# Kernel tuning notes

Measured on AMD Instinct MI355X. Metric: run time of the kernel, lower is better.

Reference implementation:

```python
import jax, jax.numpy as jnp
import numpy as np

ITEM_NUM = 100000
H = 128          # hidden_size
L_PROTO = 500    # number of prototypes
K = 4            # top-k prototypes
SEQ = 50         # max_seq_length
B = 1024
TAO = 0.1
LAMBDA = 0.1
EPS = 1e-5


def layer_norm(x, g, b):
    mu = jnp.mean(x, axis=-1, keepdims=True)
    var = jnp.mean((x - mu) ** 2, axis=-1, keepdims=True)
    return (x - mu) * jax.lax.rsqrt(var + EPS) * g + b


def setup_inputs() -> dict:
    key = jax.random.key(0)
    ks = jax.random.split(key, 12)
    std = 0.02
    item_emb = jax.random.normal(ks[0], (ITEM_NUM, H), jnp.float32) * std
    item_emb = item_emb.at[0].set(0.0)  # padding_idx=0
    pos_emb = jax.random.normal(ks[1], (SEQ + 1, H), jnp.float32) * std
    pos_emb = pos_emb.at[0].set(0.0)    # padding_idx=0 (never hit when len==SEQ)
    proto = jax.random.normal(ks[2], (L_PROTO, H), jnp.float32) * std
    w1 = jax.random.normal(ks[3], (H, H), jnp.float32) * std
    w2 = jax.random.normal(ks[4], (H, 1), jnp.float32) * std
    w3 = jax.random.normal(ks[5], (H, H), jnp.float32) * std
    w4 = jax.random.normal(ks[6], (H, H), jnp.float32) * std
    w5 = jax.random.normal(ks[7], (H, K), jnp.float32) * std
    w6 = jax.random.normal(ks[8], (H, H), jnp.float32) * std
    w7 = jax.random.normal(ks[9], (H, 1), jnp.float32) * std
    seq = jax.random.randint(ks[10], (B, SEQ), 0, ITEM_NUM, dtype=jnp.int64)
    g = jnp.ones((H,), jnp.float32)
    b = jnp.zeros((H,), jnp.float32)
    return {
        'item_emb': item_emb, 'pos_emb': pos_emb, 'proto': proto,
        'w1': w1, 'w2': w2, 'w3': w3, 'w4': w4, 'w5': w5, 'w6': w6, 'w7': w7,
        'ln1_g': g, 'ln1_b': b, 'ln2_g': g, 'ln2_b': b,
        'ln3_g': g, 'ln3_b': b, 'ln4_g': g, 'ln4_b': b,
        'seq': seq,
    }


def reference(item_emb, pos_emb, proto, w1, w2, w3, w4, w5, w6, w7,
              ln1_g, ln1_b, ln2_g, ln2_b, ln3_g, ln3_b, ln4_g, ln4_b, seq):
    mask = (seq != 0).astype(jnp.float32)            # [B,S]
    ie = item_emb[seq]                               # [B,S,H]

    # self-attentive virtual concept vector
    sa_score = jnp.squeeze(jnp.tanh(ie @ w1) @ w2, -1)   # [B,S]
    sa_score = sa_score - (1.0 - mask) * 10000.0
    alpha = jax.nn.softmax(sa_score, axis=-1)
    vcv = jnp.einsum('bs,bsh->bh', alpha, ie)            # [B,H]

    # prototype routing: top-k by score
    s = vcv @ proto.T                                    # [B,L]
    chosen_s, rank = jax.lax.top_k(s, K)                 # [B,K]
    chosen_proto = proto[rank]                           # [B,K,H]
    chosen_proto = jax.nn.sigmoid(chosen_s)[..., None] * chosen_proto

    # item->prototype assignment
    p_kt_score = jnp.einsum('bsh,bkh->bsk',
                            layer_norm(ie @ w3, ln1_g, ln1_b),
                            layer_norm(chosen_proto, ln2_g, ln2_b))
    p_kt = jax.nn.softmax(p_kt_score, axis=-1) * mask[:, :, None]  # [B,S,K]

    # positional embedding (positions SEQ..1)
    position = SEQ - jnp.arange(SEQ)                     # [S]
    emb = pos_emb[position][None, :, :] + ie             # [B,S,H]

    a_k_score = jnp.swapaxes(jnp.tanh(emb @ w4) @ w5, 1, 2)   # [B,K,S]
    a_k = jax.nn.softmax(a_k_score, axis=-1) * mask[:, None, :]
    a_k = jnp.swapaxes(a_k, 1, 2)                        # [B,S,K]

    p = p_kt * a_k
    interesting = layer_norm(jnp.einsum('bsk,bsh->bkh', p, emb), ln3_g, ln3_b)  # [B,K,H]

    xu = jnp.einsum('bsk,bkh->bsh', p_kt, chosen_proto)  # [B,S,H]
    c_score = jnp.squeeze(jnp.tanh(xu @ w6) @ w7, -1) - (1.0 - mask) * 10000.0
    c_w = jax.nn.softmax(c_score, axis=-1)               # [B,S]
    c_apt = layer_norm(jnp.einsum('bs,bsh->bh', c_w, xu), ln4_g, ln4_b)  # [B,H]

    e_score = jnp.einsum('bh,bkh->bk', c_apt, interesting)
    e = jax.nn.softmax(e_score / TAO, axis=-1)
    final = jnp.einsum('bk,bkh->bh', e, interesting)     # [B,H]
    scores = final @ item_emb.T                          # [B,ITEM_NUM]

    # prototype covariance regularizer
    centered = proto - jnp.mean(proto, axis=0, keepdims=True)
    M = (centered @ centered.T) / H
    Lc = (jnp.linalg.norm(M) - jnp.linalg.norm(jnp.diag(M))) * 0.5
    return scores, LAMBDA * Lc
```

## Files before the change

kernel.cpp:

```cpp
#include <hip/hip_runtime.h>
#include <hip/hip_bf16.h>

#define H 128
#define H2 132
#define SQL 50
#define LPROTO 500
#define KTOP 4
#define BQ 1024
#define ITEMS 100000

typedef __attribute__((ext_vector_type(8))) short bf16x8;
typedef __attribute__((ext_vector_type(4))) float f32x4;

__device__ __forceinline__ float wsum(float v){
#pragma unroll
  for (int o = 32; o; o >>= 1) v += __shfl_xor(v, o, 64);
  return v;
}
__device__ __forceinline__ float wmax(float v){
#pragma unroll
  for (int o = 32; o; o >>= 1) v = fmaxf(v, __shfl_xor(v, o, 64));
  return v;
}
__device__ __forceinline__ float gr16(float v){
  v += __shfl_xor(v, 1, 64);
  v += __shfl_xor(v, 2, 64);
  v += __shfl_xor(v, 4, 64);
  v += __shfl_xor(v, 8, 64);
  return v;
}
__device__ __forceinline__ unsigned short f2bf(float x){
  unsigned int u = __builtin_bit_cast(unsigned int, x);
  unsigned int r = u + 0x7fffu + ((u >> 16) & 1u);
  return (unsigned short)(r >> 16);
}
__device__ __forceinline__ float bf2f(unsigned short h){
  unsigned int u = ((unsigned int)h) << 16;
  return __builtin_bit_cast(float, u);
}

__device__ __forceinline__ void mm_core(const float xs[4][8],
                                        const unsigned short* __restrict__ wt_hi,
                                        const unsigned short* __restrict__ wt_lo,
                                        int r15, int kof, f32x4* acc)
{
  bf16x8 ah[4], al[4];
#pragma unroll
  for (int ks = 0; ks < 4; ks++){
    bf16x8 h, l;
#pragma unroll
    for (int e = 0; e < 8; e++){
      unsigned short hb = f2bf(xs[ks][e]);
      float rem = xs[ks][e] - bf2f(hb);
      h[e] = (short)hb;
      l[e] = (short)f2bf(rem);
    }
    ah[ks] = h; al[ks] = l;
  }
#pragma unroll
  for (int j = 0; j < 8; j++){
    const unsigned short* bp = wt_hi + (j * 16 + r15) * H + kof;
    const unsigned short* lp = wt_lo + (j * 16 + r15) * H + kof;
    f32x4 a = (f32x4){0.f, 0.f, 0.f, 0.f};
#pragma unroll
    for (int ks = 0; ks < 4; ks++){
      bf16x8 bh = *reinterpret_cast<const bf16x8*>(bp + ks * 32);
      bf16x8 bl = *reinterpret_cast<const bf16x8*>(lp + ks * 32);
      a = __builtin_amdgcn_mfma_f32_16x16x32_bf16(ah[ks], bh, a, 0, 0, 0);
      a = __builtin_amdgcn_mfma_f32_16x16x32_bf16(al[ks], bh, a, 0, 0, 0);
      a = __builtin_amdgcn_mfma_f32_16x16x32_bf16(ah[ks], bl, a, 0, 0, 0);
    }
    acc[j] = a;
  }
}

__device__ __forceinline__ void mm_acc(const float (*src)[H2],
                                       const unsigned short* __restrict__ wt_hi,
                                       const unsigned short* __restrict__ wt_lo,
                                       int lane, int wave, f32x4* acc)
{
  const int r15 = lane & 15, g = lane >> 4, kof = g * 8;
  const int row = wave * 16 + r15;
  const int srw = (row < SQL) ? row : 0;
  float xs[4][8];
#pragma unroll
  for (int ks = 0; ks < 4; ks++){
    const float* p = &src[srw][ks * 32 + kof];
    float4 x0 = *reinterpret_cast<const float4*>(p);
    float4 x1 = *reinterpret_cast<const float4*>(p + 4);
    xs[ks][0]=x0.x; xs[ks][1]=x0.y; xs[ks][2]=x0.z; xs[ks][3]=x0.w;
    xs[ks][4]=x1.x; xs[ks][5]=x1.y; xs[ks][6]=x1.z; xs[ks][7]=x1.w;
  }
  mm_core(xs, wt_hi, wt_lo, r15, kof, acc);
}

__device__ __forceinline__ void mm_acc_pos(const float (*src)[H2],
                                           const float* __restrict__ pos_emb,
                                           const unsigned short* __restrict__ wt_hi,
                                           const unsigned short* __restrict__ wt_lo,
                                           int lane, int wave, f32x4* acc)
{
  const int r15 = lane & 15, g = lane >> 4, kof = g * 8;
  const int row = wave * 16 + r15;
  const int srw = (row < SQL) ? row : 0;
  const float* pp = pos_emb + (SQL - srw) * H;
  float xs[4][8];
#pragma unroll
  for (int ks = 0; ks < 4; ks++){
    const float* p = &src[srw][ks * 32 + kof];
    float4 x0 = *reinterpret_cast<const float4*>(p);
    float4 x1 = *reinterpret_cast<const float4*>(p + 4);
    float4 p0 = *reinterpret_cast<const float4*>(pp + ks * 32 + kof);
    float4 p1 = *reinterpret_cast<const float4*>(pp + ks * 32 + kof + 4);
    xs[ks][0]=x0.x+p0.x; xs[ks][1]=x0.y+p0.y; xs[ks][2]=x0.z+p0.z; xs[ks][3]=x0.w+p0.w;
    xs[ks][4]=x1.x+p1.x; xs[ks][5]=x1.y+p1.y; xs[ks][6]=x1.z+p1.z; xs[ks][7]=x1.w+p1.w;
  }
  mm_core(xs, wt_hi, wt_lo, r15, kof, acc);
}

extern "C" __global__ __launch_bounds__(256, 4)
void sine_row(const float* __restrict__ item_emb, const float* __restrict__ pos_emb,
              const float* __restrict__ proto,
              const float* __restrict__ w2, const float* __restrict__ w5,
              const float* __restrict__ w7,
              const unsigned short* __restrict__ wt,
              const float* __restrict__ ln1g, const float* __restrict__ ln1b,
              const float* __restrict__ ln2g, const float* __restrict__ ln2b,
              const float* __restrict__ ln3g, const float* __restrict__ ln3b,
              const float* __restrict__ ln4g, const float* __restrict__ ln4b,
              const int* __restrict__ seq,
              unsigned short* __restrict__ finalbf)
{
  __shared__ __align__(16) float sA[SQL][H2];
  __shared__ __align__(16) float scp[KTOP][H];
  __shared__ __align__(16) float slncp[KTOP][H];
  __shared__ __align__(16) float sintr[KTOP][H];
  __shared__ __align__(16) float svcv[H];
  __shared__ __align__(16) float scapt[H];
  __shared__ float srow[SQL];
  __shared__ float smask[SQL];
  __shared__ float spkt[SQL][KTOP];
  __shared__ float sak[SQL][KTOP];
  __shared__ float ssc[LPROTO];
  __shared__ float schs[KTOP];
  __shared__ int   srank[KTOP];
  __shared__ float sesc[KTOP];

  const int b = blockIdx.x;
  const int t = threadIdx.x;
  const int lane = t & 63;
  const int wave = t >> 6;
  const int r15 = lane & 15;
  const int g   = lane >> 4;
  const int* sq = seq + b * SQL;

  const unsigned short* w1t_hi = wt;
  const unsigned short* w1t_lo = wt + 16384;
  const unsigned short* w3t_hi = wt + 32768;
  const unsigned short* w3t_lo = wt + 49152;
  const unsigned short* w4t_hi = wt + 65536;
  const unsigned short* w4t_lo = wt + 81920;
  const unsigned short* w6t_hi = wt + 98304;
  const unsigned short* w6t_lo = wt + 114688;

  if (t < SQL) smask[t] = (sq[t] != 0) ? 1.0f : 0.0f;
  for (int c = t; c < SQL * (H / 4); c += 256){
    int s = c >> 5, q = c & 31;
    int idx = sq[s];
    float4 v = reinterpret_cast<const float4*>(item_emb)[idx * (H / 4) + q];
    reinterpret_cast<float4*>(&sA[s][0])[q] = v;
  }
  __syncthreads();

  {
    f32x4 acc[8];
    mm_acc(sA, w1t_hi, w1t_lo, lane, wave, acc);
    float p0 = 0.f, p1 = 0.f, p2 = 0.f, p3 = 0.f;
#pragma unroll
    for (int j = 0; j < 8; j++){
      float w2c = w2[j * 16 + r15];
      p0 = fmaf(tanhf(acc[j][0]), w2c, p0);
      p1 = fmaf(tanhf(acc[j][1]), w2c, p1);
      p2 = fmaf(tanhf(acc[j][2]), w2c, p2);
      p3 = fmaf(tanhf(acc[j][3]), w2c, p3);
    }
    p0 = gr16(p0); p1 = gr16(p1); p2 = gr16(p2); p3 = gr16(p3);
    if (r15 == 0){
      float pv[4] = {p0, p1, p2, p3};
#pragma unroll
      for (int r = 0; r < 4; r++){
        int orow = wave * 16 + g * 4 + r;
        if (orow < SQL) srow[orow] = pv[r] - (1.0f - smask[orow]) * 10000.0f;
      }
    }
  }
  __syncthreads();

  if (wave == 0){
    float v = (lane < SQL) ? srow[lane] : -1e30f;
    float m = wmax(v);
    float e = (lane < SQL) ? expf(v - m) : 0.0f;
    float sum = wsum(e);
    if (lane < SQL) srow[lane] = e / sum;
  }
  __syncthreads();
  if (t < H){
    float acc = 0.f;
    for (int s = 0; s < SQL; s++) acc = fmaf(srow[s], sA[s][t], acc);
    svcv[t] = acc;
  }
  __syncthreads();

  for (int l = t; l < LPROTO; l += 256){
    const float4* pr = reinterpret_cast<const float4*>(proto + l * H);
    const float4* vc = reinterpret_cast<const float4*>(svcv);
    float acc = 0.f;
    for (int q = 0; q < H / 4; q++){
      float4 p = pr[q], v = vc[q];
      acc += p.x * v.x + p.y * v.y + p.z * v.z + p.w * v.w;
    }
    ssc[l] = acc;
  }
  __syncthreads();
  if (wave == 0){
    float cand[8];
#pragma unroll
    for (int i = 0; i < 8; i++){
      int l = lane + 64 * i;
      cand[i] = (l < LPROTO) ? ssc[l] : -1e30f;
    }
    for (int k = 0; k < KTOP; k++){
      float bv = -1e30f; int bi = 0x7fffffff;
#pragma unroll
      for (int i = 0; i < 8; i++){
        int l = lane + 64 * i;
        if (cand[i] > bv || (cand[i] == bv && l < bi)){ bv = cand[i]; bi = l; }
      }
#pragma unroll
      for (int o = 32; o; o >>= 1){
        float ov = __shfl_xor(bv, o, 64);
        int   oi = __shfl_xor(bi, o, 64);
        if (ov > bv || (ov == bv && oi < bi)){ bv = ov; bi = oi; }
      }
      if (lane == 0){ schs[k] = bv; srank[k] = bi; }
      int li = bi - lane;
#pragma unroll
      for (int i = 0; i < 8; i++) if (64 * i == li) cand[i] = -1e30f;
    }
  }
  __syncthreads();
  {
    int k = wave;
    int r = srank[k];
    float sg = 1.0f / (1.0f + expf(-schs[k]));
    float v0 = sg * proto[r * H + lane];
    float v1 = sg * proto[r * H + 64 + lane];
    float mu = wsum(v0 + v1) * (1.0f / H);
    float d0 = v0 - mu, d1 = v1 - mu;
    float var = wsum(d0 * d0 + d1 * d1) * (1.0f / H);
    float rs = rsqrtf(var + 1e-5f);
    scp[k][lane] = v0; scp[k][64 + lane] = v1;
    slncp[k][lane]      = d0 * rs * ln2g[lane]      + ln2b[lane];
    slncp[k][64 + lane] = d1 * rs * ln2g[64 + lane] + ln2b[64 + lane];
  }
  __syncthreads();

  {
    f32x4 acc[8];
    mm_acc(sA, w3t_hi, w3t_lo, lane, wave, acc);
    float s0 = 0.f, s1 = 0.f, s2 = 0.f, s3 = 0.f;
#pragma unroll
    for (int j = 0; j < 8; j++){ s0 += acc[j][0]; s1 += acc[j][1]; s2 += acc[j][2]; s3 += acc[j][3]; }
    float mu0 = gr16(s0) * (1.0f / H), mu1 = gr16(s1) * (1.0f / H);
    float mu2 = gr16(s2) * (1.0f / H), mu3 = gr16(s3) * (1.0f / H);
    float q0 = 0.f, q1 = 0.f, q2 = 0.f, q3 = 0.f;
#pragma unroll
    for (int j = 0; j < 8; j++){
      float d0 = acc[j][0] - mu0, d1 = acc[j][1] - mu1;
      float d2 = acc[j][2] - mu2, d3 = acc[j][3] - mu3;
      q0 = fmaf(d0, d0, q0); q1 = fmaf(d1, d1, q1);
      q2 = fmaf(d2, d2, q2); q3 = fmaf(d3, d3, q3);
    }
    float rs0 = rsqrtf(gr16(q0) * (1.0f / H) + 1e-5f);
    float rs1 = rsqrtf(gr16(q1) * (1.0f / H) + 1e-5f);
    float rs2 = rsqrtf(gr16(q2) * (1.0f / H) + 1e-5f);
    float rs3 = rsqrtf(gr16(q3) * (1.0f / H) + 1e-5f);
    float pk[4][4];
#pragma unroll
    for (int k = 0; k < 4; k++)
#pragma unroll
      for (int r = 0; r < 4; r++) pk[k][r] = 0.f;
#pragma unroll
    for (int j = 0; j < 8; j++){
      int c = j * 16 + r15;
      float gg = ln1g[c], bb = ln1b[c];
      float l0 = fmaf((acc[j][0] - mu0) * rs0, gg, bb);
      float l1 = fmaf((acc[j][1] - mu1) * rs1, gg, bb);
      float l2 = fmaf((acc[j][2] - mu2) * rs2, gg, bb);
      float l3 = fmaf((acc[j][3] - mu3) * rs3, gg, bb);
#pragma unroll
      for (int k = 0; k < 4; k++){
        float w = slncp[k][c];
        pk[k][0] = fmaf(l0, w, pk[k][0]);
        pk[k][1] = fmaf(l1, w, pk[k][1]);
        pk[k][2] = fmaf(l2, w, pk[k][2]);
        pk[k][3] = fmaf(l3, w, pk[k][3]);
      }
    }
#pragma unroll
    for (int k = 0; k < 4; k++)
#pragma unroll
      for (int r = 0; r < 4; r++) pk[k][r] = gr16(pk[k][r]);
    if (r15 == 0){
#pragma unroll
      for (int r = 0; r < 4; r++){
        int orow = wave * 16 + g * 4 + r;
        if (orow < SQL){
          float m = fmaxf(fmaxf(pk[0][r], pk[1][r]), fmaxf(pk[2][r], pk[3][r]));
          float e0 = expf(pk[0][r] - m), e1 = expf(pk[1][r] - m);
          float e2 = expf(pk[2][r] - m), e3 = expf(pk[3][r] - m);
          float inv = 1.0f / (e0 + e1 + e2 + e3);
          float msk = smask[orow];
          spkt[orow][0] = e0 * inv * msk; spkt[orow][1] = e1 * inv * msk;
          spkt[orow][2] = e2 * inv * msk; spkt[orow][3] = e3 * inv * msk;
        }
      }
    }
  }
  __syncthreads();

  {
    f32x4 acc[8];
    mm_acc_pos(sA, pos_emb, w4t_hi, w4t_lo, lane, wave, acc);
    float pk[4][4];
#pragma unroll
    for (int k = 0; k < 4; k++)
#pragma unroll
      for (int r = 0; r < 4; r++) pk[k][r] = 0.f;
#pragma unroll
    for (int j = 0; j < 8; j++){
      int c = j * 16 + r15;
      float4 w5c = *reinterpret_cast<const float4*>(w5 + c * 4);
      float t0 = tanhf(acc[j][0]), t1 = tanhf(acc[j][1]);
      float t2 = tanhf(acc[j][2]), t3 = tanhf(acc[j][3]);
      pk[0][0] = fmaf(t0, w5c.x, pk[0][0]); pk[0][1] = fmaf(t1, w5c.x, pk[0][1]);
      pk[0][2] = fmaf(t2, w5c.x, pk[0][2]); pk[0][3] = fmaf(t3, w5c.x, pk[0][3]);
      pk[1][0] = fmaf(t0, w5c.y, pk[1][0]); pk[1][1] = fmaf(t1, w5c.y, pk[1][1]);
      pk[1][2] = fmaf(t2, w5c.y, pk[1][2]); pk[1][3] = fmaf(t3, w5c.y, pk[1][3]);
      pk[2][0] = fmaf(t0, w5c.z, pk[2][0]); pk[2][1] = fmaf(t1, w5c.z, pk[2][1]);
      pk[2][2] = fmaf(t2, w5c.z, pk[2][2]); pk[2][3] = fmaf(t3, w5c.z, pk[2][3]);
      pk[3][0] = fmaf(t0, w5c.w, pk[3][0]); pk[3][1] = fmaf(t1, w5c.w, pk[3][1]);
      pk[3][2] = fmaf(t2, w5c.w, pk[3][2]); pk[3][3] = fmaf(t3, w5c.w, pk[3][3]);
    }
#pragma unroll
    for (int k = 0; k < 4; k++)
#pragma unroll
      for (int r = 0; r < 4; r++) pk[k][r] = gr16(pk[k][r]);
    if (r15 == 0){
#pragma unroll
      for (int r = 0; r < 4; r++){
        int orow = wave * 16 + g * 4 + r;
        if (orow < SQL){
          sak[orow][0] = pk[0][r]; sak[orow][1] = pk[1][r];
          sak[orow][2] = pk[2][r]; sak[orow][3] = pk[3][r];
        }
      }
    }
  }
  __syncthreads();

  {
    int k = wave;
    float v = (lane < SQL) ? sak[lane][k] : -1e30f;
    float m = wmax(v);
    float e = (lane < SQL) ? expf(v - m) : 0.0f;
    float sum = wsum(e);
    if (lane < SQL) sak[lane][k] = (e / sum) * smask[lane] * spkt[lane][k];
  }
  __syncthreads();

  for (int c = t; c < KTOP * H; c += 256){
    int k = c >> 7, h = c & 127;
    float acc = 0.f;
    for (int s = 0; s < SQL; s++)
      acc = fmaf(sak[s][k], sA[s][h] + pos_emb[(SQL - s) * H + h], acc);
    sintr[k][h] = acc;
  }
  __syncthreads();
  {
    int k = wave;
    float v0 = sintr[k][lane], v1 = sintr[k][64 + lane];
    float mu = wsum(v0 + v1) * (1.0f / H);
    float d0 = v0 - mu, d1 = v1 - mu;
    float var = wsum(d0 * d0 + d1 * d1) * (1.0f / H);
    float rs = rsqrtf(var + 1e-5f);
    sintr[k][lane]      = d0 * rs * ln3g[lane]      + ln3b[lane];
    sintr[k][64 + lane] = d1 * rs * ln3g[64 + lane] + ln3b[64 + lane];
  }
  __syncthreads();

  for (int c = t; c < SQL * H; c += 256){
    int s = c >> 7, h = c & 127;
    float acc = spkt[s][0] * scp[0][h] + spkt[s][1] * scp[1][h]
              + spkt[s][2] * scp[2][h] + spkt[s][3] * scp[3][h];
    sA[s][h] = acc;
  }
  __syncthreads();
  {
    f32x4 acc[8];
    mm_acc(sA, w6t_hi, w6t_lo, lane, wave, acc);
    float p0 = 0.f, p1 = 0.f, p2 = 0.f, p3 = 0.f;
#pragma unroll
    for (int j = 0; j < 8; j++){
      float w7c = w7[j * 16 + r15];
      p0 = fmaf(tanhf(acc[j][0]), w7c, p0);
      p1 = fmaf(tanhf(acc[j][1]), w7c, p1);
      p2 = fmaf(tanhf(acc[j][2]), w7c, p2);
      p3 = fmaf(tanhf(acc[j][3]), w7c, p3);
    }
    p0 = gr16(p0); p1 = gr16(p1); p2 = gr16(p2); p3 = gr16(p3);
    if (r15 == 0){
      float pv[4] = {p0, p1, p2, p3};
#pragma unroll
      for (int r = 0; r < 4; r++){
        int orow = wave * 16 + g * 4 + r;
        if (orow < SQL) srow[orow] = pv[r] - (1.0f - smask[orow]) * 10000.0f;
      }
    }
  }
  __syncthreads();

  if (wave == 0){
    float v = (lane < SQL) ? srow[lane] : -1e30f;
    float m = wmax(v);
    float e = (lane < SQL) ? expf(v - m) : 0.0f;
    float sum = wsum(e);
    if (lane < SQL) srow[lane] = e / sum;
  }
  __syncthreads();
  if (t < H){
    float acc = 0.f;
    for (int s = 0; s < SQL; s++) acc = fmaf(srow[s], sA[s][t], acc);
    scapt[t] = acc;
  }
  __syncthreads();
  if (wave == 0){
    float v0 = scapt[lane], v1 = scapt[64 + lane];
    float mu = wsum(v0 + v1) * (1.0f / H);
    float d0 = v0 - mu, d1 = v1 - mu;
    float var = wsum(d0 * d0 + d1 * d1) * (1.0f / H);
    float rs = rsqrtf(var + 1e-5f);
    scapt[lane]      = d0 * rs * ln4g[lane]      + ln4b[lane];
    scapt[64 + lane] = d1 * rs * ln4g[64 + lane] + ln4b[64 + lane];
  }
  __syncthreads();

  {
    int k = wave;
    float part = scapt[lane] * sintr[k][lane] + scapt[64 + lane] * sintr[k][64 + lane];
    float sc = wsum(part);
    if (lane == 0) sesc[k] = sc;
  }
  __syncthreads();
  if (t < H){
    float e0 = sesc[0] * 10.0f, e1 = sesc[1] * 10.0f, e2 = sesc[2] * 10.0f, e3 = sesc[3] * 10.0f;
    float m = fmaxf(fmaxf(e0, e1), fmaxf(e2, e3));
    float x0 = expf(e0 - m), x1 = expf(e1 - m), x2 = expf(e2 - m), x3 = expf(e3 - m);
    float inv = 1.0f / (x0 + x1 + x2 + x3);
    float f = (x0 * sintr[0][t] + x1 * sintr[1][t] + x2 * sintr[2][t] + x3 * sintr[3][t]) * inv;
    finalbf[b * H + t] = f2bf(f);
  }
}

extern "C" __global__ void wprep(const float* __restrict__ w1, const float* __restrict__ w3,
                                 const float* __restrict__ w4, const float* __restrict__ w6,
                                 unsigned short* __restrict__ out){
  const float* srcs[4] = {w1, w3, w4, w6};
  const float* src = srcs[blockIdx.x];
  unsigned short* hi = out + blockIdx.x * 32768;
  unsigned short* lo = hi + 16384;
  for (int i = threadIdx.x; i < 16384; i += 256){
    int c = i >> 7, k = i & 127;
    float f = src[k * H + c];
    unsigned short h = f2bf(f);
    hi[i] = h;
    lo[i] = f2bf(f - bf2f(h));
  }
}

extern "C" __global__ void conv_bf16(const float* __restrict__ in,
                                     unsigned short* __restrict__ out, int n4){
  int i = blockIdx.x * blockDim.x + threadIdx.x;
  int stride = gridDim.x * blockDim.x;
  for (; i < n4; i += stride){
    float4 v = reinterpret_cast<const float4*>(in)[i];
    union { unsigned short u[4]; uint2 v2; } o;
    o.u[0] = f2bf(v.x); o.u[1] = f2bf(v.y); o.u[2] = f2bf(v.z); o.u[3] = f2bf(v.w);
    reinterpret_cast<uint2*>(out)[i] = o.v2;
  }
}

#define GBM 128
#define GBN 128
#define LDT 136

extern "C" __global__ __launch_bounds__(256)
void gemm_scores(const unsigned short* __restrict__ A,
                 const unsigned short* __restrict__ Bm,
                 float* __restrict__ C)
{
  __shared__ __align__(16) unsigned short sA[GBM][LDT];
  __shared__ __align__(16) unsigned short sB[GBN][LDT];
  const int t = threadIdx.x, lane = t & 63, wave = t >> 6;
  const int r15 = lane & 15, g = lane >> 4;
  const int n0 = blockIdx.x * GBN;
  const int m0 = blockIdx.y * GBM;

  for (int c = t; c < GBM * 16; c += 256){
    int r = c >> 4, q = c & 15;
    uint4 v = reinterpret_cast<const uint4*>(A + (m0 + r) * H)[q];
    *reinterpret_cast<uint4*>(&sA[r][q * 8]) = v;
  }
  for (int c = t; c < GBN * 16; c += 256){
    int r = c >> 4, q = c & 15;
    int n = n0 + r;
    uint4 v = make_uint4(0u, 0u, 0u, 0u);
    if (n < ITEMS) v = reinterpret_cast<const uint4*>(Bm + (size_t)n * H)[q];
    *reinterpret_cast<uint4*>(&sB[r][q * 8]) = v;
  }
  __syncthreads();

  const int wm = wave >> 1, wn = wave & 1;
  f32x4 acc[4][4];
#pragma unroll
  for (int i = 0; i < 4; i++)
#pragma unroll
    for (int j = 0; j < 4; j++) acc[i][j] = (f32x4){0.f, 0.f, 0.f, 0.f};

#pragma unroll
  for (int ks = 0; ks < 4; ks++){
    bf16x8 af[4], bfr[4];
#pragma unroll
    for (int i = 0; i < 4; i++)
      af[i] = *reinterpret_cast<const bf16x8*>(&sA[wm * 64 + i * 16 + r15][ks * 32 + g * 8]);
#pragma unroll
    for (int j = 0; j < 4; j++)
      bfr[j] = *reinterpret_cast<const bf16x8*>(&sB[wn * 64 + j * 16 + r15][ks * 32 + g * 8]);
#pragma unroll
    for (int i = 0; i < 4; i++)
#pragma unroll
      for (int j = 0; j < 4; j++)
        acc[i][j] = __builtin_amdgcn_mfma_f32_16x16x32_bf16(af[i], bfr[j], acc[i][j], 0, 0, 0);
  }

#pragma unroll
  for (int i = 0; i < 4; i++){
    int mrow = m0 + wm * 64 + i * 16 + g * 4;
#pragma unroll
    for (int j = 0; j < 4; j++){
      int ncol = n0 + wn * 64 + j * 16 + r15;
      if (ncol < ITEMS){
#pragma unroll
        for (int r = 0; r < 4; r++)
          C[(size_t)(mrow + r) * ITEMS + ncol] = acc[i][j][r];
      }
    }
  }
}

extern "C" __global__ void proto_mean(const float* __restrict__ proto,
                                      float* __restrict__ mean, float* __restrict__ accum){
  int h = threadIdx.x;
  if (h < 2) accum[h] = 0.0f;
  float acc = 0.f;
  for (int l = 0; l < LPROTO; l++) acc += proto[l * H + h];
  mean[h] = acc * (1.0f / LPROTO);
}

extern "C" __global__ __launch_bounds__(256)
void proto_cov(const float* __restrict__ proto, const float* __restrict__ mean,
               float* __restrict__ accum){
  __shared__ float ci[H];
  __shared__ float red[256];
  int i = blockIdx.x, t = threadIdx.x;
  if (t < H) ci[t] = proto[i * H + t] - mean[t];
  __syncthreads();
  float total = 0.f;
  for (int j = t; j < LPROTO; j += 256){
    float acc = 0.f;
    for (int h = 0; h < H; h++) acc = fmaf(ci[h], proto[j * H + h] - mean[h], acc);
    float m = acc * (1.0f / H);
    total += m * m;
    if (j == i) atomicAdd(&accum[1], m * m);
  }
  red[t] = total; __syncthreads();
  for (int o = 128; o; o >>= 1){ if (t < o) red[t] += red[t + o]; __syncthreads(); }
  if (t == 0) atomicAdd(&accum[0], red[0]);
}

extern "C" __global__ void lc_final(const float* __restrict__ accum, float* __restrict__ out){
  out[(size_t)BQ * ITEMS] = 0.1f * 0.5f * (sqrtf(accum[0]) - sqrtf(accum[1]));
}

extern "C" void kernel_launch(void* const* d_in, const int* in_sizes, int n_in,
                              void* d_out, int out_size, void* d_ws, size_t ws_size,
                              hipStream_t stream){
  const float* item  = (const float*)d_in[0];
  const float* pos   = (const float*)d_in[1];
  const float* proto = (const float*)d_in[2];
  const float* w1 = (const float*)d_in[3];
  const float* w2 = (const float*)d_in[4];
  const float* w3 = (const float*)d_in[5];
  const float* w4 = (const float*)d_in[6];
  const float* w5 = (const float*)d_in[7];
  const float* w6 = (const float*)d_in[8];
  const float* w7 = (const float*)d_in[9];
  const float* ln1g = (const float*)d_in[10];
  const float* ln1b = (const float*)d_in[11];
  const float* ln2g = (const float*)d_in[12];
  const float* ln2b = (const float*)d_in[13];
  const float* ln3g = (const float*)d_in[14];
  const float* ln3b = (const float*)d_in[15];
  const float* ln4g = (const float*)d_in[16];
  const float* ln4b = (const float*)d_in[17];
  const int* seq = (const int*)d_in[18];
  float* out = (float*)d_out;

  char* ws = (char*)d_ws;
  float* accum = (float*)ws;
  float* mean  = (float*)(ws + 256);
  unsigned short* finalbf = (unsigned short*)(ws + 1024);
  unsigned short* itembf  = (unsigned short*)(ws + 263168);
  unsigned short* wtbuf   = (unsigned short*)(ws + 25863168);

  wprep<<<4, 256, 0, stream>>>(w1, w3, w4, w6, wtbuf);
  conv_bf16<<<2048, 256, 0, stream>>>(item, itembf, ITEMS * H / 4);

  sine_row<<<BQ, 256, 0, stream>>>(item, pos, proto, w2, w5, w7, wtbuf,
                                   ln1g, ln1b, ln2g, ln2b, ln3g, ln3b, ln4g, ln4b,
                                   seq, finalbf);

  gemm_scores<<<dim3((ITEMS + GBN - 1) / GBN, BQ / GBM), 256, 0, stream>>>(finalbf, itembf, out);

  proto_mean<<<1, 128, 0, stream>>>(proto, mean, accum);
  proto_cov<<<LPROTO, 256, 0, stream>>>(proto, mean, accum);
  lc_final<<<1, 1, 0, stream>>>(accum, out);
}
```

Measured before the change: 366.0 us.

## Stream all query rows per item tile in score GEMM; use fast exp/tanh

The score GEMM now runs one block per 128-item tile and loops over all 1024 query rows inside the block. Each item tile is staged in shared memory once instead of once per 128-row query tile, and the A fragments are read straight from global memory. Separately, tanhf/expf in the row kernel are swapped for __expf-based fast versions, proto_mean is parallelized across 512 threads, and the mean is cached in shared memory in proto_cov. The risks are a grid of only ~782 blocks, each doing long serial work, and A reads that go through global/L2 instead of LDS.

```diff
diff --git a/kernel.cpp b/kernel.cpp
--- a/kernel.cpp
+++ b/kernel.cpp
@@ -37,6 +37,11 @@
 __device__ __forceinline__ float bf2f(unsigned short h){
   unsigned int u = ((unsigned int)h) << 16;
   return __builtin_bit_cast(float, u);
+}
+__device__ __forceinline__ float ftanh(float x){
+  float e = __expf(-2.0f * fabsf(x));
+  float t = (1.0f - e) / (1.0f + e);
+  return copysignf(t, x);
 }
 
 __device__ __forceinline__ void mm_core(const float xs[4][8],
@@ -179,10 +184,10 @@
 #pragma unroll
     for (int j = 0; j < 8; j++){
       float w2c = w2[j * 16 + r15];
-      p0 = fmaf(tanhf(acc[j][0]), w2c, p0);
-      p1 = fmaf(tanhf(acc[j][1]), w2c, p1);
-      p2 = fmaf(tanhf(acc[j][2]), w2c, p2);
-      p3 = fmaf(tanhf(acc[j][3]), w2c, p3);
+      p0 = fmaf(ftanh(acc[j][0]), w2c, p0);
+      p1 = fmaf(ftanh(acc[j][1]), w2c, p1);
+      p2 = fmaf(ftanh(acc[j][2]), w2c, p2);
+      p3 = fmaf(ftanh(acc[j][3]), w2c, p3);
     }
     p0 = gr16(p0); p1 = gr16(p1); p2 = gr16(p2); p3 = gr16(p3);
     if (r15 == 0){
@@ -199,7 +204,7 @@
   if (wave == 0){
     float v = (lane < SQL) ? srow[lane] : -1e30f;
     float m = wmax(v);
-    float e = (lane < SQL) ? expf(v - m) : 0.0f;
+    float e = (lane < SQL) ? __expf(v - m) : 0.0f;
     float sum = wsum(e);
     if (lane < SQL) srow[lane] = e / sum;
   }
@@ -252,7 +257,7 @@
   {
     int k = wave;
     int r = srank[k];
-    float sg = 1.0f / (1.0f + expf(-schs[k]));
+    float sg = 1.0f / (1.0f + __expf(-schs[k]));
     float v0 = sg * proto[r * H + lane];
     float v1 = sg * proto[r * H + 64 + lane];
     float mu = wsum(v0 + v1) * (1.0f / H);
@@ -317,8 +322,8 @@
         int orow = wave * 16 + g * 4 + r;
         if (orow < SQL){
           float m = fmaxf(fmaxf(pk[0][r], pk[1][r]), fmaxf(pk[2][r], pk[3][r]));
-          float e0 = expf(pk[0][r] - m), e1 = expf(pk[1][r] - m);
-          float e2 = expf(pk[2][r] - m), e3 = expf(pk[3][r] - m);
+          float e0 = __expf(pk[0][r] - m), e1 = __expf(pk[1][r] - m);
+          float e2 = __expf(pk[2][r] - m), e3 = __expf(pk[3][r] - m);
           float inv = 1.0f / (e0 + e1 + e2 + e3);
           float msk = smask[orow];
           spkt[orow][0] = e0 * inv * msk; spkt[orow][1] = e1 * inv * msk;
@@ -341,8 +346,8 @@
     for (int j = 0; j < 8; j++){
       int c = j * 16 + r15;
       float4 w5c = *reinterpret_cast<const float4*>(w5 + c * 4);
-      float t0 = tanhf(acc[j][0]), t1 = tanhf(acc[j][1]);
-      float t2 = tanhf(acc[j][2]), t3 = tanhf(acc[j][3]);
+      float t0 = ftanh(acc[j][0]), t1 = ftanh(acc[j][1]);
+      float t2 = ftanh(acc[j][2]), t3 = ftanh(acc[j][3]);
       pk[0][0] = fmaf(t0, w5c.x, pk[0][0]); pk[0][1] = fmaf(t1, w5c.x, pk[0][1]);
       pk[0][2] = fmaf(t2, w5c.x, pk[0][2]); pk[0][3] = fmaf(t3, w5c.x, pk[0][3]);
       pk[1][0] = fmaf(t0, w5c.y, pk[1][0]); pk[1][1] = fmaf(t1, w5c.y, pk[1][1]);
@@ -373,7 +378,7 @@
     int k = wave;
     float v = (lane < SQL) ? sak[lane][k] : -1e30f;
     float m = wmax(v);
-    float e = (lane < SQL) ? expf(v - m) : 0.0f;
+    float e = (lane < SQL) ? __expf(v - m) : 0.0f;
     float sum = wsum(e);
     if (lane < SQL) sak[lane][k] = (e / sum) * smask[lane] * spkt[lane][k];
   }
@@ -413,10 +418,10 @@
 #pragma unroll
     for (int j = 0; j < 8; j++){
       float w7c = w7[j * 16 + r15];
-      p0 = fmaf(tanhf(acc[j][0]), w7c, p0);
-      p1 = fmaf(tanhf(acc[j][1]), w7c, p1);
-      p2 = fmaf(tanhf(acc[j][2]), w7c, p2);
-      p3 = fmaf(tanhf(acc[j][3]), w7c, p3);
+      p0 = fmaf(ftanh(acc[j][0]), w7c, p0);
+      p1 = fmaf(ftanh(acc[j][1]), w7c, p1);
+      p2 = fmaf(ftanh(acc[j][2]), w7c, p2);
+      p3 = fmaf(ftanh(acc[j][3]), w7c, p3);
     }
     p0 = gr16(p0); p1 = gr16(p1); p2 = gr16(p2); p3 = gr16(p3);
     if (r15 == 0){
@@ -433,7 +438,7 @@
   if (wave == 0){
     float v = (lane < SQL) ? srow[lane] : -1e30f;
     float m = wmax(v);
-    float e = (lane < SQL) ? expf(v - m) : 0.0f;
+    float e = (lane < SQL) ? __expf(v - m) : 0.0f;
     float sum = wsum(e);
     if (lane < SQL) srow[lane] = e / sum;
   }
@@ -465,7 +470,7 @@
   if (t < H){
     float e0 = sesc[0] * 10.0f, e1 = sesc[1] * 10.0f, e2 = sesc[2] * 10.0f, e3 = sesc[3] * 10.0f;
     float m = fmaxf(fmaxf(e0, e1), fmaxf(e2, e3));
-    float x0 = expf(e0 - m), x1 = expf(e1 - m), x2 = expf(e2 - m), x3 = expf(e3 - m);
+    float x0 = __expf(e0 - m), x1 = __expf(e1 - m), x2 = __expf(e2 - m), x3 = __expf(e3 - m);
     float inv = 1.0f / (x0 + x1 + x2 + x3);
     float f = (x0 * sintr[0][t] + x1 * sintr[1][t] + x2 * sintr[2][t] + x3 * sintr[3][t]) * inv;
     finalbf[b * H + t] = f2bf(f);
@@ -500,7 +505,6 @@
   }
 }
 
-#define GBM 128
 #define GBN 128
 #define LDT 136
 
@@ -509,18 +513,11 @@
                  const unsigned short* __restrict__ Bm,
                  float* __restrict__ C)
 {
-  __shared__ __align__(16) unsigned short sA[GBM][LDT];
   __shared__ __align__(16) unsigned short sB[GBN][LDT];
   const int t = threadIdx.x, lane = t & 63, wave = t >> 6;
   const int r15 = lane & 15, g = lane >> 4;
   const int n0 = blockIdx.x * GBN;
-  const int m0 = blockIdx.y * GBM;
-
-  for (int c = t; c < GBM * 16; c += 256){
-    int r = c >> 4, q = c & 15;
-    uint4 v = reinterpret_cast<const uint4*>(A + (m0 + r) * H)[q];
-    *reinterpret_cast<uint4*>(&sA[r][q * 8]) = v;
-  }
+
   for (int c = t; c < GBN * 16; c += 256){
     int r = c >> 4, q = c & 15;
     int n = n0 + r;
@@ -530,39 +527,39 @@
   }
   __syncthreads();
 
-  const int wm = wave >> 1, wn = wave & 1;
-  f32x4 acc[4][4];
-#pragma unroll
-  for (int i = 0; i < 4; i++)
-#pragma unroll
-    for (int j = 0; j < 4; j++) acc[i][j] = (f32x4){0.f, 0.f, 0.f, 0.f};
-
-#pragma unroll
-  for (int ks = 0; ks < 4; ks++){
-    bf16x8 af[4], bfr[4];
-#pragma unroll
-    for (int i = 0; i < 4; i++)
-      af[i] = *reinterpret_cast<const bf16x8*>(&sA[wm * 64 + i * 16 + r15][ks * 32 + g * 8]);
-#pragma unroll
-    for (int j = 0; j < 4; j++)
-      bfr[j] = *reinterpret_cast<const bf16x8*>(&sB[wn * 64 + j * 16 + r15][ks * 32 + g * 8]);
-#pragma unroll
-    for (int i = 0; i < 4; i++)
-#pragma unroll
-      for (int j = 0; j < 4; j++)
-        acc[i][j] = __builtin_amdgcn_mfma_f32_16x16x32_bf16(af[i], bfr[j], acc[i][j], 0, 0, 0);
-  }
-
-#pragma unroll
-  for (int i = 0; i < 4; i++){
-    int mrow = m0 + wm * 64 + i * 16 + g * 4;
-#pragma unroll
-    for (int j = 0; j < 4; j++){
-      int ncol = n0 + wn * 64 + j * 16 + r15;
-      if (ncol < ITEMS){
-#pragma unroll
-        for (int r = 0; r < 4; r++)
-          C[(size_t)(mrow + r) * ITEMS + ncol] = acc[i][j][r];
+  for (int mt = 0; mt < BQ / 128; mt++){
+    const int m0 = mt * 128 + wave * 32;
+    f32x4 acc[2][8];
+#pragma unroll
+    for (int i = 0; i < 2; i++)
+#pragma unroll
+      for (int j = 0; j < 8; j++) acc[i][j] = (f32x4){0.f, 0.f, 0.f, 0.f};
+
+#pragma unroll
+    for (int ks = 0; ks < 4; ks++){
+      bf16x8 af[2];
+#pragma unroll
+      for (int i = 0; i < 2; i++)
+        af[i] = *reinterpret_cast<const bf16x8*>(A + (m0 + i * 16 + r15) * H + ks * 32 + g * 8);
+#pragma unroll
+      for (int j = 0; j < 8; j++){
+        bf16x8 bfr = *reinterpret_cast<const bf16x8*>(&sB[j * 16 + r15][ks * 32 + g * 8]);
+        acc[0][j] = __builtin_amdgcn_mfma_f32_16x16x32_bf16(af[0], bfr, acc[0][j], 0, 0, 0);
+        acc[1][j] = __builtin_amdgcn_mfma_f32_16x16x32_bf16(af[1], bfr, acc[1][j], 0, 0, 0);
+      }
+    }
+
+#pragma unroll
+    for (int i = 0; i < 2; i++){
+      int mrow = m0 + i * 16 + g * 4;
+#pragma unroll
+      for (int j = 0; j < 8; j++){
+        int nc = n0 + j * 16 + r15;
+        if (nc < ITEMS){
+#pragma unroll
+          for (int r = 0; r < 4; r++)
+            C[(size_t)(mrow + r) * ITEMS + nc] = acc[i][j][r];
+        }
       }
     }
   }
@@ -570,25 +567,30 @@
 
 extern "C" __global__ void proto_mean(const float* __restrict__ proto,
                                       float* __restrict__ mean, float* __restrict__ accum){
-  int h = threadIdx.x;
-  if (h < 2) accum[h] = 0.0f;
+  __shared__ float part[4][H];
+  int t = threadIdx.x;
+  int h = t & 127, p = t >> 7;
+  if (t < 2) accum[t] = 0.0f;
   float acc = 0.f;
-  for (int l = 0; l < LPROTO; l++) acc += proto[l * H + h];
-  mean[h] = acc * (1.0f / LPROTO);
+  for (int l = p; l < LPROTO; l += 4) acc += proto[l * H + h];
+  part[p][h] = acc;
+  __syncthreads();
+  if (t < H) mean[t] = (part[0][t] + part[1][t] + part[2][t] + part[3][t]) * (1.0f / LPROTO);
 }
 
 extern "C" __global__ __launch_bounds__(256)
 void proto_cov(const float* __restrict__ proto, const float* __restrict__ mean,
                float* __restrict__ accum){
   __shared__ float ci[H];
+  __shared__ float cm[H];
   __shared__ float red[256];
   int i = blockIdx.x, t = threadIdx.x;
-  if (t < H) ci[t] = proto[i * H + t] - mean[t];
+  if (t < H){ cm[t] = mean[t]; ci[t] = proto[i * H + t] - mean[t]; }
   __syncthreads();
   float total = 0.f;
   for (int j = t; j < LPROTO; j += 256){
     float acc = 0.f;
-    for (int h = 0; h < H; h++) acc = fmaf(ci[h], proto[j * H + h] - mean[h], acc);
+    for (int h = 0; h < H; h++) acc = fmaf(ci[h], proto[j * H + h] - cm[h], acc);
     float m = acc * (1.0f / H);
     total += m * m;
     if (j == i) atomicAdd(&accum[1], m * m);
@@ -640,9 +642,9 @@
                                    ln1g, ln1b, ln2g, ln2b, ln3g, ln3b, ln4g, ln4b,
                                    seq, finalbf);
 
-  gemm_scores<<<dim3((ITEMS + GBN - 1) / GBN, BQ / GBM), 256, 0, stream>>>(finalbf, itembf, out);
-
-  proto_mean<<<1, 128, 0, stream>>>(proto, mean, accum);
+  gemm_scores<<<dim3((ITEMS + GBN - 1) / GBN), 256, 0, stream>>>(finalbf, itembf, out);
+
+  proto_mean<<<1, 512, 0, stream>>>(proto, mean, accum);
   proto_cov<<<LPROTO, 256, 0, stream>>>(proto, mean, accum);
   lc_final<<<1, 1, 0, stream>>>(accum, out);
 }
```

Result: slower. 390.4 us (+6.7%).
